# Kernel optimization log

Measured on AMD Instinct MI355X. Metric: run time of the kernel, lower is better.

The kernel has to match this reference:

```python
import math
import jax, jax.numpy as jnp
import numpy as np

B, S, D = 2, 2048, 1024
N_HEADS, D_KV = 16, 64
INNER = N_HEADS * D_KV
NUM_BUCKETS = 32
MAX_DISTANCE = 128


def _relative_position_bucket(relative_position, num_buckets=NUM_BUCKETS, max_distance=MAX_DISTANCE):
    # bidirectional (encoder) variant
    nb = num_buckets // 2
    rel_buckets = (relative_position > 0).astype(jnp.int32) * nb
    rp = jnp.abs(relative_position)
    max_exact = nb // 2
    is_small = rp < max_exact
    rp_safe = jnp.maximum(rp, 1)  # avoid log(0); selected away by where
    rp_if_large = max_exact + (
        jnp.log(rp_safe.astype(jnp.float32) / max_exact)
        / math.log(max_distance / max_exact)
        * (nb - max_exact)
    ).astype(jnp.int32)
    rp_if_large = jnp.minimum(rp_if_large, nb - 1)
    return rel_buckets + jnp.where(is_small, rp, rp_if_large)


def compute_bias(rel_bias, q_len, k_len):
    ctx = jnp.arange(q_len)[:, None]
    mem = jnp.arange(k_len)[None, :]
    buckets = _relative_position_bucket(mem - ctx)  # [q_len, k_len]
    values = rel_bias[buckets]                      # [q_len, k_len, H]
    return jnp.transpose(values, (2, 0, 1))[None]   # [1, H, q_len, k_len]


def setup_inputs() -> dict:
    key = jax.random.key(0)
    ks = jax.random.split(key, 6)
    s = 1.0 / math.sqrt(D)
    return {
        "hidden_states": jax.random.normal(ks[0], (B, S, D), jnp.float32),
        "wq": jax.random.normal(ks[1], (D, INNER), jnp.float32) * s,
        "wk": jax.random.normal(ks[2], (D, INNER), jnp.float32) * s,
        "wv": jax.random.normal(ks[3], (D, INNER), jnp.float32) * s,
        "wo": jax.random.normal(ks[4], (INNER, D), jnp.float32) * s,
        "rel_bias": jax.random.normal(ks[5], (NUM_BUCKETS, N_HEADS), jnp.float32) * 0.1,
    }


def reference(hidden_states, wq, wk, wv, wo, rel_bias):
    b, s, _ = hidden_states.shape

    def shape(x):  # [b, s, inner] -> [b, h, s, d_kv]
        return x.reshape(b, s, N_HEADS, D_KV).transpose(0, 2, 1, 3)

    q = shape(hidden_states @ wq)  # note: T5 has NO 1/sqrt(d) scaling
    k = shape(hidden_states @ wk)
    v = shape(hidden_states @ wv)

    scores = jnp.einsum("bhqd,bhkd->bhqk", q, k)
    position_bias = compute_bias(rel_bias, s, s)
    scores = scores + position_bias
    attn = jax.nn.softmax(scores.astype(jnp.float32), axis=-1).astype(scores.dtype)

    out = jnp.einsum("bhqk,bhkd->bhqd", attn, v)
    out = out.transpose(0, 2, 1, 3).reshape(b, s, INNER)
    return out @ wo
```

## Files before the change

### kernel.cpp

```cpp
#include <hip/hip_runtime.h>
#include <hip/hip_bf16.h>

#define B_ 2
#define S_ 2048
#define D_ 1024
#define H_ 16
#define DKV_ 64
#define INNER_ 1024
#define M_ (B_*S_)

typedef unsigned short ushort_t;
typedef unsigned int u32;
typedef __bf16 bf16x8 __attribute__((ext_vector_type(8)));
typedef __bf16 bf16x4 __attribute__((ext_vector_type(4)));
typedef float f32x4 __attribute__((ext_vector_type(4)));

#define VMCNT0 asm volatile("s_waitcnt vmcnt(0)" ::: "memory")
#define LOG2E 1.4426950408889634f

__device__ __forceinline__ unsigned short f2bf(float f) {
    unsigned int u = __builtin_bit_cast(unsigned int, f);
    unsigned int r = (u + 0x7fffu + ((u >> 16) & 1u)) >> 16;
    return (unsigned short)r;
}

__device__ __forceinline__ void gload16(const ushort_t* g, ushort_t* l) {
    __builtin_amdgcn_global_load_lds(
        (const __attribute__((address_space(1))) u32*)g,
        (__attribute__((address_space(3))) u32*)l, 16, 0, 0);
}

__global__ __launch_bounds__(256) void prep_kernel(
        const float* __restrict__ hs,
        const float* __restrict__ s0, const float* __restrict__ s1,
        const float* __restrict__ s2, const float* __restrict__ s3,
        const float* __restrict__ rb,
        unsigned short* __restrict__ Abf,
        unsigned short* __restrict__ d0, unsigned short* __restrict__ d1,
        unsigned short* __restrict__ d2, unsigned short* __restrict__ d3,
        float* __restrict__ btab) {
    int bid = blockIdx.x, tid = threadIdx.x;
    if (bid < 4096) {
        int i = (bid * 256 + tid) * 4;
        float4 v = *(const float4*)&hs[i];
        ushort4 o;
        o.x = f2bf(v.x); o.y = f2bf(v.y); o.z = f2bf(v.z); o.w = f2bf(v.w);
        *(ushort4*)&Abf[i] = o;
    } else if (bid < 5120) {
        int t = bid - 4096;
        int z = t >> 8, rem = t & 255;
        int k0 = ((rem >> 4) & 15) * 64, n0 = (rem & 15) * 64;
        const float* srcs[4] = {s0, s1, s2, s3};
        unsigned short* dsts[4] = {d0, d1, d2, d3};
        const float* src = srcs[z];
        unsigned short* dst = dsts[z];
        __shared__ float tbuf[64][65];
        for (int i = tid; i < 4096; i += 256) {
            int r = i >> 6, c = i & 63;
            tbuf[r][c] = src[(k0 + r) * 1024 + n0 + c];
        }
        __syncthreads();
        for (int i = tid; i < 4096; i += 256) {
            int r = i >> 6, c = i & 63;
            dst[(n0 + r) * 1024 + k0 + c] = f2bf(tbuf[c][r]);
        }
    } else {
        #pragma unroll
        for (int j = 0; j < 4; ++j) {
            int idx = (bid - 5120) * 1024 + j * 256 + tid;
            int h = idx >> 12, pos = idx & 4095;
            int rel = pos - 2048;
            int bb = rel > 0 ? 16 : 0;
            int rp = rel < 0 ? -rel : rel;
            int bucket;
            if (rp < 8) bucket = bb + rp;
            else {
                int v = 8 + (int)(logf((float)rp * 0.125f) / 2.7725887f * 8.0f);
                bucket = bb + (v < 15 ? v : 15);
            }
            btab[idx] = rb[bucket * 16 + h] * LOG2E;
        }
    }
}

__global__ __launch_bounds__(256) void gemm_qkv(const ushort_t* __restrict__ A,
        const ushort_t* __restrict__ WQ, const ushort_t* __restrict__ WK, const ushort_t* __restrict__ WV,
        ushort_t* __restrict__ Qb, ushort_t* __restrict__ Kb, ushort_t* __restrict__ Vtb) {
    __shared__ alignas(16) ushort_t As[128][64];
    __shared__ alignas(16) ushort_t Bs[128][64];
    int tid = threadIdx.x, wid = tid >> 6, lane = tid & 63;
    int linear = blockIdx.x;
    int swz = (linear & 7) * 96 + (linear >> 3);
    int m0 = (swz / 24) * 128;
    int nblk = swz % 24;
    int sel = nblk >> 3;
    const ushort_t* Bt = sel == 0 ? WQ : (sel == 1 ? WK : WV);
    int n0 = (nblk & 7) * 128;
    int lr = lane & 15, lg = lane >> 4;
    int wm = (wid >> 1) * 64, wn = (wid & 1) * 64;
    int srow = tid >> 3, sp = tid & 7;
    int scol = (sp ^ (srow & 7)) * 8;
    int cR0 = (lg ^ (lr & 7)) * 8;
    int cR1 = ((4 + lg) ^ (lr & 7)) * 8;
    const ushort_t* Abase = A + (size_t)m0 * 1024 + scol;
    const ushort_t* Bbase = Bt + (size_t)n0 * 1024 + scol;
    f32x4 acc[4][4] = {};
    for (int kt = 0; kt < 1024; kt += 64) {
        #pragma unroll
        for (int j = 0; j < 4; ++j) {
            int row = j * 32 + srow;
            gload16(Abase + row * 1024 + kt, &As[0][0] + (j * 256 + tid) * 8);
            gload16(Bbase + row * 1024 + kt, &Bs[0][0] + (j * 256 + tid) * 8);
        }
        VMCNT0;
        __syncthreads();
        bf16x8 af[4][2], bfr[4][2];
        #pragma unroll
        for (int t = 0; t < 4; ++t) {
            af[t][0]  = *(const bf16x8*)&As[wm + t * 16 + lr][cR0];
            af[t][1]  = *(const bf16x8*)&As[wm + t * 16 + lr][cR1];
            bfr[t][0] = *(const bf16x8*)&Bs[wn + t * 16 + lr][cR0];
            bfr[t][1] = *(const bf16x8*)&Bs[wn + t * 16 + lr][cR1];
        }
        #pragma unroll
        for (int hh = 0; hh < 2; ++hh)
            #pragma unroll
            for (int i2 = 0; i2 < 4; ++i2)
                #pragma unroll
                for (int j2 = 0; j2 < 4; ++j2)
                    acc[i2][j2] = __builtin_amdgcn_mfma_f32_16x16x32_bf16(af[i2][hh], bfr[j2][hh], acc[i2][j2], 0, 0, 0);
        __syncthreads();
    }
    #pragma unroll
    for (int i2 = 0; i2 < 4; ++i2)
        #pragma unroll
        for (int j2 = 0; j2 < 4; ++j2) {
            int col = n0 + wn + j2 * 16 + lr;
            int hh = col >> 6, d = col & 63;
            if (sel < 2) {
                ushort_t* dst = sel == 0 ? Qb : Kb;
                #pragma unroll
                for (int r = 0; r < 4; ++r) {
                    int row = m0 + wm + i2 * 16 + lg * 4 + r;
                    int b = row >> 11, s = row & 2047;
                    dst[(((size_t)(b * H_ + hh) * S_ + s)) * DKV_ + d] = f2bf(acc[i2][j2][r]);
                }
            } else {
                int row0 = m0 + wm + i2 * 16 + lg * 4;
                int b = row0 >> 11, s0 = row0 & 2047;
                ushort4 sv;
                sv.x = f2bf(acc[i2][j2][0]); sv.y = f2bf(acc[i2][j2][1]);
                sv.z = f2bf(acc[i2][j2][2]); sv.w = f2bf(acc[i2][j2][3]);
                *(ushort4*)&Vtb[((size_t)(b * H_ + hh) * DKV_ + d) * S_ + s0] = sv;
            }
        }
}

__global__ __launch_bounds__(256) void gemm_out(const ushort_t* __restrict__ A,
                                                const ushort_t* __restrict__ Bt,
                                                float* __restrict__ C) {
    __shared__ alignas(16) ushort_t As[64][64];
    __shared__ alignas(16) ushort_t Bs[128][64];
    int tid = threadIdx.x, wid = tid >> 6, lane = tid & 63;
    int linear = blockIdx.x;
    int swz = (linear & 7) * 64 + (linear >> 3);
    int m0 = (swz >> 3) * 64, n0 = (swz & 7) * 128;
    int lr = lane & 15, lg = lane >> 4;
    int wn = wid * 32;
    int srow = tid >> 3, sp = tid & 7;
    int scol = (sp ^ (srow & 7)) * 8;
    int cR0 = (lg ^ (lr & 7)) * 8;
    int cR1 = ((4 + lg) ^ (lr & 7)) * 8;
    const ushort_t* Abase = A + (size_t)m0 * 1024 + scol;
    const ushort_t* Bbase = Bt + (size_t)n0 * 1024 + scol;
    f32x4 acc[4][2] = {};
    for (int kt = 0; kt < 1024; kt += 64) {
        #pragma unroll
        for (int j = 0; j < 2; ++j) {
            int row = j * 32 + srow;
            gload16(Abase + row * 1024 + kt, &As[0][0] + (j * 256 + tid) * 8);
        }
        #pragma unroll
        for (int j = 0; j < 4; ++j) {
            int row = j * 32 + srow;
            gload16(Bbase + row * 1024 + kt, &Bs[0][0] + (j * 256 + tid) * 8);
        }
        VMCNT0;
        __syncthreads();
        bf16x8 af[4][2], bfr[2][2];
        #pragma unroll
        for (int t = 0; t < 4; ++t) {
            af[t][0] = *(const bf16x8*)&As[t * 16 + lr][cR0];
            af[t][1] = *(const bf16x8*)&As[t * 16 + lr][cR1];
        }
        #pragma unroll
        for (int j = 0; j < 2; ++j) {
            bfr[j][0] = *(const bf16x8*)&Bs[wn + j * 16 + lr][cR0];
            bfr[j][1] = *(const bf16x8*)&Bs[wn + j * 16 + lr][cR1];
        }
        #pragma unroll
        for (int hh = 0; hh < 2; ++hh)
            #pragma unroll
            for (int i2 = 0; i2 < 4; ++i2)
                #pragma unroll
                for (int j2 = 0; j2 < 2; ++j2)
                    acc[i2][j2] = __builtin_amdgcn_mfma_f32_16x16x32_bf16(af[i2][hh], bfr[j2][hh], acc[i2][j2], 0, 0, 0);
        __syncthreads();
    }
    #pragma unroll
    for (int i2 = 0; i2 < 4; ++i2)
        #pragma unroll
        for (int j2 = 0; j2 < 2; ++j2)
            #pragma unroll
            for (int r = 0; r < 4; ++r)
                C[(size_t)(m0 + i2 * 16 + lg * 4 + r) * 1024 + n0 + wn + j2 * 16 + lr] = acc[i2][j2][r];
}

__global__ __launch_bounds__(256, 2) void flash_attn(const ushort_t* __restrict__ Q,
                                                     const ushort_t* __restrict__ Kg,
                                                     const ushort_t* __restrict__ Vt,
                                                     const float* __restrict__ bias_tab,
                                                     ushort_t* __restrict__ Out) {
    __shared__ alignas(16) ushort_t Ks[2][64][64];
    __shared__ alignas(16) ushort_t Ps[4][16][64];
    __shared__ float LbS[2176];
    int tid = threadIdx.x, wid = tid >> 6, lane = tid & 63;
    int linear = blockIdx.x;
    int swz = (linear & 7) * 64 + (linear >> 3);
    int bh = swz >> 4, qblk = swz & 15;
    int h = bh & 15, b = bh >> 4;
    int q0b = qblk * 128;
    int q0w = q0b + wid * 32;
    int lr = lane & 15, lg = lane >> 4;

    {
        const float* bsrc = bias_tab + h * 4096 + 2048 - q0b - 127;
        for (int i = tid; i < 2175; i += 256) LbS[i] = bsrc[i];
    }
    float cpos = bias_tab[h * 4096 + 4095];
    float cneg = bias_tab[h * 4096 + 0];

    const ushort_t* Qbase = Q + ((size_t)bh * S_ + q0w) * DKV_;
    bf16x8 qA0 = *(const bf16x8*)&Qbase[lr * DKV_ + lg * 8];
    bf16x8 qA1 = *(const bf16x8*)&Qbase[lr * DKV_ + 32 + lg * 8];
    bf16x8 qB0 = *(const bf16x8*)&Qbase[(16 + lr) * DKV_ + lg * 8];
    bf16x8 qB1 = *(const bf16x8*)&Qbase[(16 + lr) * DKV_ + 32 + lg * 8];

    int srow = tid >> 3, sp = tid & 7;
    int kc = (sp ^ (srow & 7)) * 8;
    const ushort_t* Ksrc = Kg + (size_t)bh * S_ * DKV_ + kc;
    const ushort_t* Vfrag = Vt + ((size_t)bh * DKV_ + lr) * S_ + lg * 8;
    int c0 = (lg ^ (lr & 7)) * 8;
    int c1 = ((4 + lg) ^ (lr & 7)) * 8;
    int pxor = (lr & 7) << 4;

    f32x4 oA[4] = {}, oB[4] = {};
    f32x4 lpA = {}, lpB = {};
    const int bbA = 127 - wid * 32 + 4 * lg - lr;
    const int bbB = bbA - 16;

    auto stageK = [&](int bi, int kt) {
        ushort_t* kb = &Ks[bi][0][0];
        gload16(Ksrc + (size_t)(kt + srow) * 64,      kb + tid * 8);
        gload16(Ksrc + (size_t)(kt + 32 + srow) * 64, kb + 2048 + tid * 8);
    };
    auto loadV = [&](int kt, bf16x8 (&v)[4][2]) {
        #pragma unroll
        for (int dt = 0; dt < 4; ++dt) {
            const ushort_t* vp = Vfrag + (size_t)dt * 16 * S_ + kt;
            v[dt][0] = *(const bf16x8*)vp;
            v[dt][1] = *(const bf16x8*)(vp + 32);
        }
    };
    auto qk = [&](int buf, f32x4* sA, f32x4* sB) {
        __builtin_amdgcn_s_setprio(1);
        #pragma unroll
        for (int nt = 0; nt < 4; ++nt) {
            bf16x8 kf0 = *(const bf16x8*)&Ks[buf][nt * 16 + lr][c0];
            bf16x8 kf1 = *(const bf16x8*)&Ks[buf][nt * 16 + lr][c1];
            sA[nt] = __builtin_amdgcn_mfma_f32_16x16x32_bf16(kf0, qA0, sA[nt], 0, 0, 0);
            sA[nt] = __builtin_amdgcn_mfma_f32_16x16x32_bf16(kf1, qA1, sA[nt], 0, 0, 0);
            sB[nt] = __builtin_amdgcn_mfma_f32_16x16x32_bf16(kf0, qB0, sB[nt], 0, 0, 0);
            sB[nt] = __builtin_amdgcn_mfma_f32_16x16x32_bf16(kf1, qB1, sB[nt], 0, 0, 0);
        }
        __builtin_amdgcn_s_setprio(0);
    };
    auto smpv = [&](f32x4 (&s)[4], f32x4& lp, f32x4 (&o)[4],
                    int bi, bool far, float cb, const bf16x8 (&vf)[4][2]) {
        float p[4][4];
        if (far) {
            #pragma unroll
            for (int nt = 0; nt < 4; ++nt)
                #pragma unroll
                for (int r = 0; r < 4; ++r)
                    p[nt][r] = __builtin_amdgcn_exp2f(fmaf(s[nt][r], LOG2E, cb));
        } else {
            #pragma unroll
            for (int nt = 0; nt < 4; ++nt)
                #pragma unroll
                for (int r = 0; r < 4; ++r)
                    p[nt][r] = __builtin_amdgcn_exp2f(fmaf(s[nt][r], LOG2E, LbS[bi + nt * 16 + r]));
        }
        char* pbase = (char*)&Ps[wid][lr][0];
        #pragma unroll
        for (int nt = 0; nt < 4; ++nt) {
            #pragma unroll
            for (int r = 0; r < 4; ++r) lp[r] += p[nt][r];
            bf16x4 pv;
            pv[0] = (__bf16)p[nt][0]; pv[1] = (__bf16)p[nt][1];
            pv[2] = (__bf16)p[nt][2]; pv[3] = (__bf16)p[nt][3];
            *(bf16x4*)(pbase + ((nt * 32 + lg * 8) ^ pxor)) = pv;
        }
        bf16x8 pf0 = *(const bf16x8*)(pbase + ((lg * 16) ^ pxor));
        bf16x8 pf1 = *(const bf16x8*)(pbase + ((64 + lg * 16) ^ pxor));
        __builtin_amdgcn_s_setprio(1);
        #pragma unroll
        for (int dt = 0; dt < 4; ++dt) {
            o[dt] = __builtin_amdgcn_mfma_f32_16x16x32_bf16(vf[dt][0], pf0, o[dt], 0, 0, 0);
            o[dt] = __builtin_amdgcn_mfma_f32_16x16x32_bf16(vf[dt][1], pf1, o[dt], 0, 0, 0);
        }
        __builtin_amdgcn_s_setprio(0);
    };

    bf16x8 vu[4][2], vn[4][2];
    f32x4 sCA[4] = {}, sCB[4] = {};

    stageK(0, 0);
    stageK(1, 64);
    loadV(0, vu);
    asm volatile("s_waitcnt vmcnt(8) lgkmcnt(0)" ::: "memory");
    __builtin_amdgcn_s_barrier();
    __builtin_amdgcn_sched_barrier(0);
    qk(0, sCA, sCB);
    __builtin_amdgcn_s_barrier();
    __builtin_amdgcn_sched_barrier(0);

    #pragma unroll 2
    for (int t = 0; t < 32; ++t) {
        const int kt = t * 64;
        const bool even = (t & 1) == 0;
        bf16x8 (&vuse)[4][2] = even ? vu : vn;
        bf16x8 (&vnxt)[4][2] = even ? vn : vu;
        if (t < 31) loadV(kt + 64, vnxt);
        if (t < 30) stageK(t & 1, kt + 128);
        __builtin_amdgcn_sched_barrier(0);
        f32x4 sNA[4] = {}, sNB[4] = {};
        if (t < 31) qk((t + 1) & 1, sNA, sNB);
        const bool far = (kt >= q0b + 256) || (kt + 64 <= q0b - 128);
        const float cb = (kt > q0b) ? cpos : cneg;
        smpv(sCA, lpA, oA, kt + bbA, far, cb, vuse);
        smpv(sCB, lpB, oB, kt + bbB, far, cb, vuse);
        #pragma unroll
        for (int nt = 0; nt < 4; ++nt) { sCA[nt] = sNA[nt]; sCB[nt] = sNB[nt]; }
        if (t < 30) {
            asm volatile("s_waitcnt vmcnt(10)" ::: "memory");
            __builtin_amdgcn_s_barrier();
            __builtin_amdgcn_sched_barrier(0);
        } else if (t == 30) {
            asm volatile("s_waitcnt vmcnt(8)" ::: "memory");
            __builtin_amdgcn_s_barrier();
            __builtin_amdgcn_sched_barrier(0);
        }
    }

    float lA = (lpA[0] + lpA[1]) + (lpA[2] + lpA[3]);
    lA += __shfl_xor(lA, 16); lA += __shfl_xor(lA, 32);
    float lB = (lpB[0] + lpB[1]) + (lpB[2] + lpB[3]);
    lB += __shfl_xor(lB, 16); lB += __shfl_xor(lB, 32);
    {
        float linv = 1.f / lA;
        char* pbase = (char*)&Ps[wid][lr][0];
        #pragma unroll
        for (int dt = 0; dt < 4; ++dt) {
            bf16x4 ov;
            ov[0] = (__bf16)(oA[dt][0] * linv); ov[1] = (__bf16)(oA[dt][1] * linv);
            ov[2] = (__bf16)(oA[dt][2] * linv); ov[3] = (__bf16)(oA[dt][3] * linv);
            *(bf16x4*)(pbase + ((dt * 32 + lg * 8) ^ pxor)) = ov;
        }
        int row = lane >> 2, seg = lane & 3;
        int rxor = (row & 7) << 4;
        char* rbase = (char*)&Ps[wid][row][0];
        uint4 v0 = *(uint4*)(rbase + ((seg * 32) ^ rxor));
        uint4 v1 = *(uint4*)(rbase + ((seg * 32 + 16) ^ rxor));
        ushort_t* dst = Out + (size_t)(b * S_ + q0w + row) * INNER_ + h * DKV_ + seg * 16;
        *(uint4*)&dst[0] = v0;
        *(uint4*)&dst[8] = v1;
    }
    {
        float linv = 1.f / lB;
        char* pbase = (char*)&Ps[wid][lr][0];
        #pragma unroll
        for (int dt = 0; dt < 4; ++dt) {
            bf16x4 ov;
            ov[0] = (__bf16)(oB[dt][0] * linv); ov[1] = (__bf16)(oB[dt][1] * linv);
            ov[2] = (__bf16)(oB[dt][2] * linv); ov[3] = (__bf16)(oB[dt][3] * linv);
            *(bf16x4*)(pbase + ((dt * 32 + lg * 8) ^ pxor)) = ov;
        }
        int row = lane >> 2, seg = lane & 3;
        int rxor = (row & 7) << 4;
        char* rbase = (char*)&Ps[wid][row][0];
        uint4 v0 = *(uint4*)(rbase + ((seg * 32) ^ rxor));
        uint4 v1 = *(uint4*)(rbase + ((seg * 32 + 16) ^ rxor));
        ushort_t* dst = Out + (size_t)(b * S_ + q0w + 16 + row) * INNER_ + h * DKV_ + seg * 16;
        *(uint4*)&dst[0] = v0;
        *(uint4*)&dst[8] = v1;
    }
}

extern "C" void kernel_launch(void* const* d_in, const int* in_sizes, int n_in,
                              void* d_out, int out_size, void* d_ws, size_t ws_size,
                              hipStream_t stream) {
    const float* hs = (const float*)d_in[0];
    const float* wq = (const float*)d_in[1];
    const float* wk = (const float*)d_in[2];
    const float* wv = (const float*)d_in[3];
    const float* wo = (const float*)d_in[4];
    const float* rb = (const float*)d_in[5];

    char* ws = (char*)d_ws;
    unsigned short* Abf = (unsigned short*)(ws);
    unsigned short* Wqt = (unsigned short*)(ws + (8u  << 20));
    unsigned short* Wkt = (unsigned short*)(ws + (10u << 20));
    unsigned short* Wvt = (unsigned short*)(ws + (12u << 20));
    unsigned short* Wot = (unsigned short*)(ws + (14u << 20));
    unsigned short* Qb  = (unsigned short*)(ws + (16u << 20));
    unsigned short* Kb  = (unsigned short*)(ws + (24u << 20));
    unsigned short* Vtb = (unsigned short*)(ws + (32u << 20));
    unsigned short* AOb = (unsigned short*)(ws + (40u << 20));
    float*          Btab = (float*)(ws + (48u << 20));

    prep_kernel<<<5184, 256, 0, stream>>>(hs, wq, wk, wv, wo, rb,
                                          Abf, Wqt, Wkt, Wvt, Wot, Btab);

    gemm_qkv<<<768, 256, 0, stream>>>(Abf, Wqt, Wkt, Wvt, Qb, Kb, Vtb);

    flash_attn<<<512, 256, 0, stream>>>(Qb, Kb, Vtb, Btab, AOb);

    gemm_out<<<512, 256, 0, stream>>>(AOb, Wot, (float*)d_out);
}
```

Measured before the change: 130.0 us.

## Halve per-wave query rows in flash attention to raise occupancy

Each wave now handles 16 query rows instead of 32, so a block covers 64 queries and the grid doubles to 1024 blocks, with launch bounds raised to 4 blocks per SM. The V fragments are no longer double-buffered in registers; V is loaded at the top of each iteration and the loop waits on vmcnt(0). The goal is to cut register pressure so more waves can hide latency. In exchange, each K tile loaded into shared memory is reused across half as many query rows, and the V loads are no longer prefetched a tile ahead, so memory latency is exposed on every iteration.

```diff
diff --git a/kernel.cpp b/kernel.cpp
--- a/kernel.cpp
+++ b/kernel.cpp
@@ -216,26 +216,26 @@
                 C[(size_t)(m0 + i2 * 16 + lg * 4 + r) * 1024 + n0 + wn + j2 * 16 + lr] = acc[i2][j2][r];
 }
 
-__global__ __launch_bounds__(256, 2) void flash_attn(const ushort_t* __restrict__ Q,
+__global__ __launch_bounds__(256, 4) void flash_attn(const ushort_t* __restrict__ Q,
                                                      const ushort_t* __restrict__ Kg,
                                                      const ushort_t* __restrict__ Vt,
                                                      const float* __restrict__ bias_tab,
                                                      ushort_t* __restrict__ Out) {
     __shared__ alignas(16) ushort_t Ks[2][64][64];
     __shared__ alignas(16) ushort_t Ps[4][16][64];
-    __shared__ float LbS[2176];
+    __shared__ float LbS[2112];
     int tid = threadIdx.x, wid = tid >> 6, lane = tid & 63;
     int linear = blockIdx.x;
-    int swz = (linear & 7) * 64 + (linear >> 3);
-    int bh = swz >> 4, qblk = swz & 15;
+    int swz = (linear & 7) * 128 + (linear >> 3);
+    int bh = swz >> 5, qblk = swz & 31;
     int h = bh & 15, b = bh >> 4;
-    int q0b = qblk * 128;
-    int q0w = q0b + wid * 32;
+    int q0b = qblk * 64;
+    int q0w = q0b + wid * 16;
     int lr = lane & 15, lg = lane >> 4;
 
     {
-        const float* bsrc = bias_tab + h * 4096 + 2048 - q0b - 127;
-        for (int i = tid; i < 2175; i += 256) LbS[i] = bsrc[i];
+        const float* bsrc = bias_tab + h * 4096 + 2048 - q0b - 63;
+        for (int i = tid; i < 2111; i += 256) LbS[i] = bsrc[i];
     }
     float cpos = bias_tab[h * 4096 + 4095];
     float cneg = bias_tab[h * 4096 + 0];
@@ -243,8 +243,6 @@
     const ushort_t* Qbase = Q + ((size_t)bh * S_ + q0w) * DKV_;
     bf16x8 qA0 = *(const bf16x8*)&Qbase[lr * DKV_ + lg * 8];
     bf16x8 qA1 = *(const bf16x8*)&Qbase[lr * DKV_ + 32 + lg * 8];
-    bf16x8 qB0 = *(const bf16x8*)&Qbase[(16 + lr) * DKV_ + lg * 8];
-    bf16x8 qB1 = *(const bf16x8*)&Qbase[(16 + lr) * DKV_ + 32 + lg * 8];
 
     int srow = tid >> 3, sp = tid & 7;
     int kc = (sp ^ (srow & 7)) * 8;
@@ -254,10 +252,9 @@
     int c1 = ((4 + lg) ^ (lr & 7)) * 8;
     int pxor = (lr & 7) << 4;
 
-    f32x4 oA[4] = {}, oB[4] = {};
-    f32x4 lpA = {}, lpB = {};
-    const int bbA = 127 - wid * 32 + 4 * lg - lr;
-    const int bbB = bbA - 16;
+    f32x4 oA[4] = {};
+    f32x4 lpA = {};
+    const int bbA = 63 - wid * 16 + 4 * lg - lr;
 
     auto stageK = [&](int bi, int kt) {
         ushort_t* kb = &Ks[bi][0][0];
@@ -272,7 +269,7 @@
             v[dt][1] = *(const bf16x8*)(vp + 32);
         }
     };
-    auto qk = [&](int buf, f32x4* sA, f32x4* sB) {
+    auto qk = [&](int buf, f32x4* sA) {
         __builtin_amdgcn_s_setprio(1);
         #pragma unroll
         for (int nt = 0; nt < 4; ++nt) {
@@ -280,8 +277,6 @@
             bf16x8 kf1 = *(const bf16x8*)&Ks[buf][nt * 16 + lr][c1];
             sA[nt] = __builtin_amdgcn_mfma_f32_16x16x32_bf16(kf0, qA0, sA[nt], 0, 0, 0);
             sA[nt] = __builtin_amdgcn_mfma_f32_16x16x32_bf16(kf1, qA1, sA[nt], 0, 0, 0);
-            sB[nt] = __builtin_amdgcn_mfma_f32_16x16x32_bf16(kf0, qB0, sB[nt], 0, 0, 0);
-            sB[nt] = __builtin_amdgcn_mfma_f32_16x16x32_bf16(kf1, qB1, sB[nt], 0, 0, 0);
         }
         __builtin_amdgcn_s_setprio(0);
     };
@@ -322,51 +317,40 @@
         __builtin_amdgcn_s_setprio(0);
     };
 
-    bf16x8 vu[4][2], vn[4][2];
-    f32x4 sCA[4] = {}, sCB[4] = {};
+    f32x4 sCA[4] = {};
 
     stageK(0, 0);
     stageK(1, 64);
-    loadV(0, vu);
-    asm volatile("s_waitcnt vmcnt(8) lgkmcnt(0)" ::: "memory");
+    asm volatile("s_waitcnt vmcnt(0) lgkmcnt(0)" ::: "memory");
     __builtin_amdgcn_s_barrier();
     __builtin_amdgcn_sched_barrier(0);
-    qk(0, sCA, sCB);
+    qk(0, sCA);
     __builtin_amdgcn_s_barrier();
     __builtin_amdgcn_sched_barrier(0);
 
     #pragma unroll 2
     for (int t = 0; t < 32; ++t) {
         const int kt = t * 64;
-        const bool even = (t & 1) == 0;
-        bf16x8 (&vuse)[4][2] = even ? vu : vn;
-        bf16x8 (&vnxt)[4][2] = even ? vn : vu;
-        if (t < 31) loadV(kt + 64, vnxt);
+        bf16x8 v[4][2];
+        loadV(kt, v);
         if (t < 30) stageK(t & 1, kt + 128);
         __builtin_amdgcn_sched_barrier(0);
-        f32x4 sNA[4] = {}, sNB[4] = {};
-        if (t < 31) qk((t + 1) & 1, sNA, sNB);
-        const bool far = (kt >= q0b + 256) || (kt + 64 <= q0b - 128);
+        f32x4 sNA[4] = {};
+        if (t < 31) qk((t + 1) & 1, sNA);
+        const bool far = (kt >= q0b + 192) || (kt + 64 <= q0b - 128);
         const float cb = (kt > q0b) ? cpos : cneg;
-        smpv(sCA, lpA, oA, kt + bbA, far, cb, vuse);
-        smpv(sCB, lpB, oB, kt + bbB, far, cb, vuse);
-        #pragma unroll
-        for (int nt = 0; nt < 4; ++nt) { sCA[nt] = sNA[nt]; sCB[nt] = sNB[nt]; }
-        if (t < 30) {
-            asm volatile("s_waitcnt vmcnt(10)" ::: "memory");
+        smpv(sCA, lpA, oA, kt + bbA, far, cb, v);
+        #pragma unroll
+        for (int nt = 0; nt < 4; ++nt) sCA[nt] = sNA[nt];
+        if (t < 31) {
+            asm volatile("s_waitcnt vmcnt(0)" ::: "memory");
             __builtin_amdgcn_s_barrier();
             __builtin_amdgcn_sched_barrier(0);
-        } else if (t == 30) {
-            asm volatile("s_waitcnt vmcnt(8)" ::: "memory");
-            __builtin_amdgcn_s_barrier();
-            __builtin_amdgcn_sched_barrier(0);
         }
     }
 
     float lA = (lpA[0] + lpA[1]) + (lpA[2] + lpA[3]);
     lA += __shfl_xor(lA, 16); lA += __shfl_xor(lA, 32);
-    float lB = (lpB[0] + lpB[1]) + (lpB[2] + lpB[3]);
-    lB += __shfl_xor(lB, 16); lB += __shfl_xor(lB, 32);
     {
         float linv = 1.f / lA;
         char* pbase = (char*)&Ps[wid][lr][0];
@@ -383,25 +367,6 @@
         uint4 v0 = *(uint4*)(rbase + ((seg * 32) ^ rxor));
         uint4 v1 = *(uint4*)(rbase + ((seg * 32 + 16) ^ rxor));
         ushort_t* dst = Out + (size_t)(b * S_ + q0w + row) * INNER_ + h * DKV_ + seg * 16;
-        *(uint4*)&dst[0] = v0;
-        *(uint4*)&dst[8] = v1;
-    }
-    {
-        float linv = 1.f / lB;
-        char* pbase = (char*)&Ps[wid][lr][0];
-        #pragma unroll
-        for (int dt = 0; dt < 4; ++dt) {
-            bf16x4 ov;
-            ov[0] = (__bf16)(oB[dt][0] * linv); ov[1] = (__bf16)(oB[dt][1] * linv);
-            ov[2] = (__bf16)(oB[dt][2] * linv); ov[3] = (__bf16)(oB[dt][3] * linv);
-            *(bf16x4*)(pbase + ((dt * 32 + lg * 8) ^ pxor)) = ov;
-        }
-        int row = lane >> 2, seg = lane & 3;
-        int rxor = (row & 7) << 4;
-        char* rbase = (char*)&Ps[wid][row][0];
-        uint4 v0 = *(uint4*)(rbase + ((seg * 32) ^ rxor));
-        uint4 v1 = *(uint4*)(rbase + ((seg * 32 + 16) ^ rxor));
-        ushort_t* dst = Out + (size_t)(b * S_ + q0w + 16 + row) * INNER_ + h * DKV_ + seg * 16;
         *(uint4*)&dst[0] = v0;
         *(uint4*)&dst[8] = v1;
     }
@@ -434,7 +399,7 @@
 
     gemm_qkv<<<768, 256, 0, stream>>>(Abf, Wqt, Wkt, Wvt, Qb, Kb, Vtb);
 
-    flash_attn<<<512, 256, 0, stream>>>(Qb, Kb, Vtb, Btab, AOb);
+    flash_attn<<<1024, 256, 0, stream>>>(Qb, Kb, Vtb, Btab, AOb);
 
     gemm_out<<<512, 256, 0, stream>>>(AOb, Wot, (float*)d_out);
 }
```

Measured after the change: 238.8 us. 83.6% more time.

## Split flash attention into single-wavefront blocks without barriers or bias staging

Applied to the files above, without the earlier changes.

Flash attention changes from 4-wave blocks sharing K tiles through LDS to 1-wave blocks of 32 query rows. Each wave stages its own K tiles, so block barriers go away and waits are per-wave vmcnt only. The LDS-staged bias window is replaced by direct global reads of the bias table. This removes barrier stalls and the bias staging prologue, at the cost of 4x more K global traffic (no sharing across waves) and uncached global bias loads in the near-diagonal region.

```diff
diff --git a/kernel.cpp b/kernel.cpp
--- a/kernel.cpp
+++ b/kernel.cpp
@@ -216,29 +216,26 @@
                 C[(size_t)(m0 + i2 * 16 + lg * 4 + r) * 1024 + n0 + wn + j2 * 16 + lr] = acc[i2][j2][r];
 }
 
-__global__ __launch_bounds__(256, 2) void flash_attn(const ushort_t* __restrict__ Q,
-                                                     const ushort_t* __restrict__ Kg,
-                                                     const ushort_t* __restrict__ Vt,
-                                                     const float* __restrict__ bias_tab,
-                                                     ushort_t* __restrict__ Out) {
+__global__ __launch_bounds__(64) void flash_attn(const ushort_t* __restrict__ Q,
+                                                 const ushort_t* __restrict__ Kg,
+                                                 const ushort_t* __restrict__ Vt,
+                                                 const float* __restrict__ bias_tab,
+                                                 ushort_t* __restrict__ Out) {
     __shared__ alignas(16) ushort_t Ks[2][64][64];
-    __shared__ alignas(16) ushort_t Ps[4][16][64];
-    __shared__ float LbS[2176];
-    int tid = threadIdx.x, wid = tid >> 6, lane = tid & 63;
+    __shared__ alignas(16) ushort_t Ps[2][16][64];
+    int lane = threadIdx.x;
     int linear = blockIdx.x;
-    int swz = (linear & 7) * 64 + (linear >> 3);
-    int bh = swz >> 4, qblk = swz & 15;
+    int swz = (linear & 7) * 256 + (linear >> 3);
+    int bh = swz >> 6, qblk = swz & 63;
     int h = bh & 15, b = bh >> 4;
-    int q0b = qblk * 128;
-    int q0w = q0b + wid * 32;
+    int q0w = qblk * 32;
     int lr = lane & 15, lg = lane >> 4;
 
-    {
-        const float* bsrc = bias_tab + h * 4096 + 2048 - q0b - 127;
-        for (int i = tid; i < 2175; i += 256) LbS[i] = bsrc[i];
-    }
-    float cpos = bias_tab[h * 4096 + 4095];
-    float cneg = bias_tab[h * 4096 + 0];
+    const float* btabh = bias_tab + h * 4096;
+    float cpos = btabh[4095];
+    float cneg = btabh[0];
+    const float* bA = btabh + 2048 + 4 * lg - lr - q0w;
+    const float* bB = bA - 16;
 
     const ushort_t* Qbase = Q + ((size_t)bh * S_ + q0w) * DKV_;
     bf16x8 qA0 = *(const bf16x8*)&Qbase[lr * DKV_ + lg * 8];
@@ -246,9 +243,9 @@
     bf16x8 qB0 = *(const bf16x8*)&Qbase[(16 + lr) * DKV_ + lg * 8];
     bf16x8 qB1 = *(const bf16x8*)&Qbase[(16 + lr) * DKV_ + 32 + lg * 8];
 
-    int srow = tid >> 3, sp = tid & 7;
-    int kc = (sp ^ (srow & 7)) * 8;
-    const ushort_t* Ksrc = Kg + (size_t)bh * S_ * DKV_ + kc;
+    int sp = lane & 7, sr8 = lane >> 3;
+    int kc = (sp ^ (sr8 & 7)) * 8;
+    const ushort_t* KsrcRow = Kg + (size_t)bh * S_ * DKV_ + sr8 * DKV_ + kc;
     const ushort_t* Vfrag = Vt + ((size_t)bh * DKV_ + lr) * S_ + lg * 8;
     int c0 = (lg ^ (lr & 7)) * 8;
     int c1 = ((4 + lg) ^ (lr & 7)) * 8;
@@ -256,13 +253,12 @@
 
     f32x4 oA[4] = {}, oB[4] = {};
     f32x4 lpA = {}, lpB = {};
-    const int bbA = 127 - wid * 32 + 4 * lg - lr;
-    const int bbB = bbA - 16;
 
     auto stageK = [&](int bi, int kt) {
         ushort_t* kb = &Ks[bi][0][0];
-        gload16(Ksrc + (size_t)(kt + srow) * 64,      kb + tid * 8);
-        gload16(Ksrc + (size_t)(kt + 32 + srow) * 64, kb + 2048 + tid * 8);
+        #pragma unroll
+        for (int j = 0; j < 8; ++j)
+            gload16(KsrcRow + (size_t)(kt + j * 8) * DKV_, kb + j * 512 + lane * 8);
     };
     auto loadV = [&](int kt, bf16x8 (&v)[4][2]) {
         #pragma unroll
@@ -285,8 +281,8 @@
         }
         __builtin_amdgcn_s_setprio(0);
     };
-    auto smpv = [&](f32x4 (&s)[4], f32x4& lp, f32x4 (&o)[4],
-                    int bi, bool far, float cb, const bf16x8 (&vf)[4][2]) {
+    auto smpv = [&](f32x4 (&s)[4], f32x4& lp, f32x4 (&o)[4], int pg,
+                    int kt, bool far, float cb, const float* bt, const bf16x8 (&vf)[4][2]) {
         float p[4][4];
         if (far) {
             #pragma unroll
@@ -299,9 +295,9 @@
             for (int nt = 0; nt < 4; ++nt)
                 #pragma unroll
                 for (int r = 0; r < 4; ++r)
-                    p[nt][r] = __builtin_amdgcn_exp2f(fmaf(s[nt][r], LOG2E, LbS[bi + nt * 16 + r]));
-        }
-        char* pbase = (char*)&Ps[wid][lr][0];
+                    p[nt][r] = __builtin_amdgcn_exp2f(fmaf(s[nt][r], LOG2E, bt[kt + nt * 16 + r]));
+        }
+        char* pbase = (char*)&Ps[pg][lr][0];
         #pragma unroll
         for (int nt = 0; nt < 4; ++nt) {
             #pragma unroll
@@ -328,11 +324,10 @@
     stageK(0, 0);
     stageK(1, 64);
     loadV(0, vu);
-    asm volatile("s_waitcnt vmcnt(8) lgkmcnt(0)" ::: "memory");
-    __builtin_amdgcn_s_barrier();
+    asm volatile("s_waitcnt vmcnt(16)" ::: "memory");
     __builtin_amdgcn_sched_barrier(0);
     qk(0, sCA, sCB);
-    __builtin_amdgcn_s_barrier();
+    asm volatile("s_waitcnt vmcnt(8)" ::: "memory");
     __builtin_amdgcn_sched_barrier(0);
 
     #pragma unroll 2
@@ -341,24 +336,19 @@
         const bool even = (t & 1) == 0;
         bf16x8 (&vuse)[4][2] = even ? vu : vn;
         bf16x8 (&vnxt)[4][2] = even ? vn : vu;
+        if (t < 30) stageK(t & 1, kt + 128);
         if (t < 31) loadV(kt + 64, vnxt);
-        if (t < 30) stageK(t & 1, kt + 128);
         __builtin_amdgcn_sched_barrier(0);
         f32x4 sNA[4] = {}, sNB[4] = {};
         if (t < 31) qk((t + 1) & 1, sNA, sNB);
-        const bool far = (kt >= q0b + 256) || (kt + 64 <= q0b - 128);
-        const float cb = (kt > q0b) ? cpos : cneg;
-        smpv(sCA, lpA, oA, kt + bbA, far, cb, vuse);
-        smpv(sCB, lpB, oB, kt + bbB, far, cb, vuse);
+        const bool far = (kt >= q0w + 192) || (kt + 64 <= q0w - 128);
+        const float cb = (kt > q0w) ? cpos : cneg;
+        smpv(sCA, lpA, oA, 0, kt, far, cb, bA, vuse);
+        smpv(sCB, lpB, oB, 1, kt, far, cb, bB, vuse);
         #pragma unroll
         for (int nt = 0; nt < 4; ++nt) { sCA[nt] = sNA[nt]; sCB[nt] = sNB[nt]; }
         if (t < 30) {
-            asm volatile("s_waitcnt vmcnt(10)" ::: "memory");
-            __builtin_amdgcn_s_barrier();
-            __builtin_amdgcn_sched_barrier(0);
-        } else if (t == 30) {
             asm volatile("s_waitcnt vmcnt(8)" ::: "memory");
-            __builtin_amdgcn_s_barrier();
             __builtin_amdgcn_sched_barrier(0);
         }
     }
@@ -369,7 +359,7 @@
     lB += __shfl_xor(lB, 16); lB += __shfl_xor(lB, 32);
     {
         float linv = 1.f / lA;
-        char* pbase = (char*)&Ps[wid][lr][0];
+        char* pbase = (char*)&Ps[0][lr][0];
         #pragma unroll
         for (int dt = 0; dt < 4; ++dt) {
             bf16x4 ov;
@@ -379,7 +369,7 @@
         }
         int row = lane >> 2, seg = lane & 3;
         int rxor = (row & 7) << 4;
-        char* rbase = (char*)&Ps[wid][row][0];
+        char* rbase = (char*)&Ps[0][row][0];
         uint4 v0 = *(uint4*)(rbase + ((seg * 32) ^ rxor));
         uint4 v1 = *(uint4*)(rbase + ((seg * 32 + 16) ^ rxor));
         ushort_t* dst = Out + (size_t)(b * S_ + q0w + row) * INNER_ + h * DKV_ + seg * 16;
@@ -388,7 +378,7 @@
     }
     {
         float linv = 1.f / lB;
-        char* pbase = (char*)&Ps[wid][lr][0];
+        char* pbase = (char*)&Ps[1][lr][0];
         #pragma unroll
         for (int dt = 0; dt < 4; ++dt) {
             bf16x4 ov;
@@ -398,7 +388,7 @@
         }
         int row = lane >> 2, seg = lane & 3;
         int rxor = (row & 7) << 4;
-        char* rbase = (char*)&Ps[wid][row][0];
+        char* rbase = (char*)&Ps[1][row][0];
         uint4 v0 = *(uint4*)(rbase + ((seg * 32) ^ rxor));
         uint4 v1 = *(uint4*)(rbase + ((seg * 32 + 16) ^ rxor));
         ushort_t* dst = Out + (size_t)(b * S_ + q0w + 16 + row) * INNER_ + h * DKV_ + seg * 16;
@@ -434,7 +424,7 @@
 
     gemm_qkv<<<768, 256, 0, stream>>>(Abf, Wqt, Wkt, Wvt, Qb, Kb, Vtb);
 
-    flash_attn<<<512, 256, 0, stream>>>(Qb, Kb, Vtb, Btab, AOb);
+    flash_attn<<<2048, 64, 0, stream>>>(Qb, Kb, Vtb, Btab, AOb);
 
     gemm_out<<<512, 256, 0, stream>>>(AOb, Wot, (float*)d_out);
 }
```

New measurement: 154.0 us. +18.4%, slower.

## Split attention key range in two and merge partial outputs in combine kernel

Applied to the files above, without the earlier changes.

The flash attention kernel now splits each query tile's key range into two halves, which doubles the grid to 1024 blocks. Each block writes its unnormalized partial output in bf16 plus its row sums of exponentials. A new combine kernel adds the two partials, divides by the total sum and writes the normalized result. The aim is more parallelism and better load balance across CUs, at the cost of an extra kernel launch, extra global traffic for the partials, and more prologue overhead per block. Storing unnormalized partials in bf16 also adds a little rounding error.

```diff
diff --git a/kernel.cpp b/kernel.cpp
--- a/kernel.cpp
+++ b/kernel.cpp
@@ -22,6 +22,9 @@
     unsigned int u = __builtin_bit_cast(unsigned int, f);
     unsigned int r = (u + 0x7fffu + ((u >> 16) & 1u)) >> 16;
     return (unsigned short)r;
+}
+__device__ __forceinline__ float bf2f(unsigned short s) {
+    return __builtin_bit_cast(float, (u32)s << 16);
 }
 
 __device__ __forceinline__ void gload16(const ushort_t* g, ushort_t* l) {
@@ -220,18 +223,23 @@
                                                      const ushort_t* __restrict__ Kg,
                                                      const ushort_t* __restrict__ Vt,
                                                      const float* __restrict__ bias_tab,
-                                                     ushort_t* __restrict__ Out) {
+                                                     ushort_t* __restrict__ Out0,
+                                                     ushort_t* __restrict__ Out1,
+                                                     float* __restrict__ L0,
+                                                     float* __restrict__ L1) {
     __shared__ alignas(16) ushort_t Ks[2][64][64];
     __shared__ alignas(16) ushort_t Ps[4][16][64];
     __shared__ float LbS[2176];
     int tid = threadIdx.x, wid = tid >> 6, lane = tid & 63;
     int linear = blockIdx.x;
-    int swz = (linear & 7) * 64 + (linear >> 3);
-    int bh = swz >> 4, qblk = swz & 15;
+    int swz = (linear & 7) * 128 + (linear >> 3);
+    int split = swz & 1, qt = swz >> 1;
+    int bh = qt >> 4, qblk = qt & 15;
     int h = bh & 15, b = bh >> 4;
     int q0b = qblk * 128;
     int q0w = q0b + wid * 32;
     int lr = lane & 15, lg = lane >> 4;
+    const int kbase = split * 1024;
 
     {
         const float* bsrc = bias_tab + h * 4096 + 2048 - q0b - 127;
@@ -325,9 +333,9 @@
     bf16x8 vu[4][2], vn[4][2];
     f32x4 sCA[4] = {}, sCB[4] = {};
 
-    stageK(0, 0);
-    stageK(1, 64);
-    loadV(0, vu);
+    stageK(0, kbase);
+    stageK(1, kbase + 64);
+    loadV(kbase, vu);
     asm volatile("s_waitcnt vmcnt(8) lgkmcnt(0)" ::: "memory");
     __builtin_amdgcn_s_barrier();
     __builtin_amdgcn_sched_barrier(0);
@@ -336,27 +344,23 @@
     __builtin_amdgcn_sched_barrier(0);
 
     #pragma unroll 2
-    for (int t = 0; t < 32; ++t) {
-        const int kt = t * 64;
+    for (int t = 0; t < 16; ++t) {
+        const int kt = kbase + t * 64;
         const bool even = (t & 1) == 0;
         bf16x8 (&vuse)[4][2] = even ? vu : vn;
         bf16x8 (&vnxt)[4][2] = even ? vn : vu;
-        if (t < 31) loadV(kt + 64, vnxt);
-        if (t < 30) stageK(t & 1, kt + 128);
+        if (t < 14) stageK(t & 1, kt + 128);
+        if (t < 15) loadV(kt + 64, vnxt);
         __builtin_amdgcn_sched_barrier(0);
         f32x4 sNA[4] = {}, sNB[4] = {};
-        if (t < 31) qk((t + 1) & 1, sNA, sNB);
+        if (t < 15) qk((t + 1) & 1, sNA, sNB);
         const bool far = (kt >= q0b + 256) || (kt + 64 <= q0b - 128);
         const float cb = (kt > q0b) ? cpos : cneg;
         smpv(sCA, lpA, oA, kt + bbA, far, cb, vuse);
         smpv(sCB, lpB, oB, kt + bbB, far, cb, vuse);
         #pragma unroll
         for (int nt = 0; nt < 4; ++nt) { sCA[nt] = sNA[nt]; sCB[nt] = sNB[nt]; }
-        if (t < 30) {
-            asm volatile("s_waitcnt vmcnt(10)" ::: "memory");
-            __builtin_amdgcn_s_barrier();
-            __builtin_amdgcn_sched_barrier(0);
-        } else if (t == 30) {
+        if (t < 14) {
             asm volatile("s_waitcnt vmcnt(8)" ::: "memory");
             __builtin_amdgcn_s_barrier();
             __builtin_amdgcn_sched_barrier(0);
@@ -367,14 +371,22 @@
     lA += __shfl_xor(lA, 16); lA += __shfl_xor(lA, 32);
     float lB = (lpB[0] + lpB[1]) + (lpB[2] + lpB[3]);
     lB += __shfl_xor(lB, 16); lB += __shfl_xor(lB, 32);
+
+    ushort_t* OutP = split == 0 ? Out0 : Out1;
+    float*    Lsel = split == 0 ? L0 : L1;
+    if (lane < 16) {
+        Lsel[bh * S_ + q0w + lane]      = lA;
+        Lsel[bh * S_ + q0w + 16 + lane] = __shfl(lB, lane, 64);
+    }
+    __builtin_amdgcn_s_barrier();
+
     {
-        float linv = 1.f / lA;
         char* pbase = (char*)&Ps[wid][lr][0];
         #pragma unroll
         for (int dt = 0; dt < 4; ++dt) {
             bf16x4 ov;
-            ov[0] = (__bf16)(oA[dt][0] * linv); ov[1] = (__bf16)(oA[dt][1] * linv);
-            ov[2] = (__bf16)(oA[dt][2] * linv); ov[3] = (__bf16)(oA[dt][3] * linv);
+            ov[0] = (__bf16)oA[dt][0]; ov[1] = (__bf16)oA[dt][1];
+            ov[2] = (__bf16)oA[dt][2]; ov[3] = (__bf16)oA[dt][3];
             *(bf16x4*)(pbase + ((dt * 32 + lg * 8) ^ pxor)) = ov;
         }
         int row = lane >> 2, seg = lane & 3;
@@ -382,18 +394,17 @@
         char* rbase = (char*)&Ps[wid][row][0];
         uint4 v0 = *(uint4*)(rbase + ((seg * 32) ^ rxor));
         uint4 v1 = *(uint4*)(rbase + ((seg * 32 + 16) ^ rxor));
-        ushort_t* dst = Out + (size_t)(b * S_ + q0w + row) * INNER_ + h * DKV_ + seg * 16;
+        ushort_t* dst = OutP + (size_t)(b * S_ + q0w + row) * INNER_ + h * DKV_ + seg * 16;
         *(uint4*)&dst[0] = v0;
         *(uint4*)&dst[8] = v1;
     }
     {
-        float linv = 1.f / lB;
         char* pbase = (char*)&Ps[wid][lr][0];
         #pragma unroll
         for (int dt = 0; dt < 4; ++dt) {
             bf16x4 ov;
-            ov[0] = (__bf16)(oB[dt][0] * linv); ov[1] = (__bf16)(oB[dt][1] * linv);
-            ov[2] = (__bf16)(oB[dt][2] * linv); ov[3] = (__bf16)(oB[dt][3] * linv);
+            ov[0] = (__bf16)oB[dt][0]; ov[1] = (__bf16)oB[dt][1];
+            ov[2] = (__bf16)oB[dt][2]; ov[3] = (__bf16)oB[dt][3];
             *(bf16x4*)(pbase + ((dt * 32 + lg * 8) ^ pxor)) = ov;
         }
         int row = lane >> 2, seg = lane & 3;
@@ -401,10 +412,31 @@
         char* rbase = (char*)&Ps[wid][row][0];
         uint4 v0 = *(uint4*)(rbase + ((seg * 32) ^ rxor));
         uint4 v1 = *(uint4*)(rbase + ((seg * 32 + 16) ^ rxor));
-        ushort_t* dst = Out + (size_t)(b * S_ + q0w + 16 + row) * INNER_ + h * DKV_ + seg * 16;
+        ushort_t* dst = OutP + (size_t)(b * S_ + q0w + 16 + row) * INNER_ + h * DKV_ + seg * 16;
         *(uint4*)&dst[0] = v0;
         *(uint4*)&dst[8] = v1;
     }
+}
+
+__global__ __launch_bounds__(256) void combine_kernel(ushort_t* __restrict__ O0,
+                                                      const ushort_t* __restrict__ O1,
+                                                      const float* __restrict__ L0,
+                                                      const float* __restrict__ L1) {
+    int row = blockIdx.x;
+    int bq = row >> 11, q = row & 2047;
+    int c = threadIdx.x * 4;
+    int h = c >> 6;
+    int bh = bq * H_ + h;
+    float li = 1.f / (L0[bh * S_ + q] + L1[bh * S_ + q]);
+    size_t off = (size_t)row * 1024 + c;
+    ushort4 a = *(const ushort4*)&O0[off];
+    ushort4 o = *(const ushort4*)&O1[off];
+    ushort4 r;
+    r.x = f2bf((bf2f(a.x) + bf2f(o.x)) * li);
+    r.y = f2bf((bf2f(a.y) + bf2f(o.y)) * li);
+    r.z = f2bf((bf2f(a.z) + bf2f(o.z)) * li);
+    r.w = f2bf((bf2f(a.w) + bf2f(o.w)) * li);
+    *(ushort4*)&O0[off] = r;
 }
 
 extern "C" void kernel_launch(void* const* d_in, const int* in_sizes, int n_in,
@@ -428,13 +460,18 @@
     unsigned short* Vtb = (unsigned short*)(ws + (32u << 20));
     unsigned short* AOb = (unsigned short*)(ws + (40u << 20));
     float*          Btab = (float*)(ws + (48u << 20));
+    unsigned short* Op1 = Abf;
+    float* L0 = (float*)(ws + (8u << 20));
+    float* L1 = (float*)(ws + (8u << 20) + (256u << 10));
 
     prep_kernel<<<5184, 256, 0, stream>>>(hs, wq, wk, wv, wo, rb,
                                           Abf, Wqt, Wkt, Wvt, Wot, Btab);
 
     gemm_qkv<<<768, 256, 0, stream>>>(Abf, Wqt, Wkt, Wvt, Qb, Kb, Vtb);
 
-    flash_attn<<<512, 256, 0, stream>>>(Qb, Kb, Vtb, Btab, AOb);
+    flash_attn<<<1024, 256, 0, stream>>>(Qb, Kb, Vtb, Btab, AOb, Op1, L0, L1);
+
+    combine_kernel<<<4096, 256, 0, stream>>>(AOb, Op1, L0, L1);
 
     gemm_out<<<512, 256, 0, stream>>>(AOb, Wot, (float*)d_out);
 }
```

After: 146.0 us. 1.12x slower.
